# Kernel tuning notes

Hardware: AMD Instinct MI355X
Metric: run time of the kernel (lower is better)

Reference implementation:

```python
import jax, jax.numpy as jnp
import numpy as np

N = 100000

def gcn_conv(x, src, dst, W, b, n):
    # x: [N, Fin]; src/dst: [E'] (self-loops already included); W: [Fin, Fout]
    h = x @ W  # [N, Fout]
    deg = jax.ops.segment_sum(jnp.ones_like(dst, dtype=h.dtype), dst, num_segments=n)  # [N]
    dinv = deg ** -0.5  # deg >= 1 due to self-loops
    norm = dinv[src] * dinv[dst]  # [E']
    msg = h[src] * norm[:, None]  # gather + scale, [E', Fout]
    out = jax.ops.segment_sum(msg, dst, num_segments=n)  # scatter-add to targets
    return out + b

def setup_inputs() -> dict:
    key = jax.random.key(0)
    k1, k2, k3, k4, k5, k6 = jax.random.split(key, 6)
    x = jax.random.normal(k1, (N, 128), dtype=jnp.float32)
    edge_index = jax.random.randint(k2, (2, 1600000), 0, N, dtype=jnp.int32)
    W1 = jax.random.normal(k3, (128, 64), dtype=jnp.float32) * 0.1
    b1 = jnp.zeros((64,), dtype=jnp.float32)
    W2 = jax.random.normal(k4, (64, 41), dtype=jnp.float32) * 0.1
    b2 = jnp.zeros((41,), dtype=jnp.float32)
    return {"x": x, "edge_index": edge_index, "W1": W1, "b1": b1, "W2": W2, "b2": b2}

def reference(x, edge_index, W1, b1, W2, b2):
    n = x.shape[0]
    loops = jnp.arange(n, dtype=edge_index.dtype)
    src = jnp.concatenate([edge_index[0], loops])  # add self-loops (PyG gcn_norm default)
    dst = jnp.concatenate([edge_index[1], loops])
    # dropout is identity in eval mode (self.training=False)
    h = gcn_conv(x, src, dst, W1, b1, n)
    h = jax.nn.relu(h)
    out = gcn_conv(h, src, dst, W2, b2, n)
    return out
```

## Files before the change

kernel.cpp:

```cpp
#include <hip/hip_runtime.h>


#define FIN 128
#define F1  64
#define F2  41
#define FP  64

#define BSH    8
#define BCAP   6144
#define NBMAX  512
#define CHUNK_P 8192

#define MT 128
#define KC 16

__device__ __forceinline__ unsigned short f2bf(float f) {
    unsigned u = __builtin_bit_cast(unsigned, f);
    u += 0x7FFFu + ((u >> 16) & 1u);
    return (unsigned short)(u >> 16);
}
__device__ __forceinline__ float bf2f(unsigned short h) {
    unsigned u = ((unsigned)h) << 16;
    return __builtin_bit_cast(float, u);
}

__global__ void k_zero(int* __restrict__ p, int n) {
    int i = blockIdx.x * blockDim.x + threadIdx.x;
    if (i < n) p[i] = 0;
}

__global__ __launch_bounds__(256) void k_part(
    const int* __restrict__ src, const int* __restrict__ dst,
    int* __restrict__ gcur, int* __restrict__ pairs, int E) {
    __shared__ int hist[NBMAX];
    __shared__ int gsh[NBMAX];
    __shared__ int lex[256];
    __shared__ int limg[CHUNK_P];
    __shared__ int lsh[CHUNK_P];
    __shared__ int stot;
    int tid = threadIdx.x;
    int e0  = blockIdx.x * CHUNK_P;
    hist[tid] = 0; hist[tid + 256] = 0;
    __syncthreads();
    for (int j = 0; j < CHUNK_P / 256; j++) {
        int e = e0 + j * 256 + tid;
        if (e < E) atomicAdd(&hist[dst[e] >> BSH], 1);
    }
    __syncthreads();
    int b0 = 2 * tid, b1 = 2 * tid + 1;
    int c0 = hist[b0], c1 = hist[b1];
    int s  = c0 + c1;
    lex[tid] = s;
    __syncthreads();
    for (int off = 1; off < 256; off <<= 1) {
        int v = lex[tid];
        int a = (tid >= off) ? lex[tid - off] : 0;
        __syncthreads();
        lex[tid] = v + a;
        __syncthreads();
    }
    int incl = lex[tid];
    if (tid == 255) stot = incl;
    int ex = incl - s;
    int l0 = ex, l1 = ex + c0;
    int g0 = c0 ? atomicAdd(&gcur[b0], c0) : 0;
    int g1 = c1 ? atomicAdd(&gcur[b1], c1) : 0;
    hist[b0] = l0; hist[b1] = l1;
    gsh[b0]  = b0 * BCAP + g0 - l0;
    gsh[b1]  = b1 * BCAP + g1 - l1;
    __syncthreads();
    for (int j = 0; j < CHUNK_P / 256; j++) {
        int e = e0 + j * 256 + tid;
        if (e < E) {
            int d = dst[e], sv = src[e];
            int b = d >> BSH;
            int p = atomicAdd(&hist[b], 1);
            limg[p] = (sv << BSH) | (d & 255);
            lsh[p]  = gsh[b];
        }
    }
    __syncthreads();
    int tot = stot;
    for (int k = tid; k < tot; k += 256)
        pairs[k + lsh[k]] = limg[k];
}

__global__ __launch_bounds__(256) void k_build(
    const int* __restrict__ gcur, const int* __restrict__ pairs,
    int* __restrict__ adjcur, int* __restrict__ adj,
    int2* __restrict__ rowinfo, float* __restrict__ dinv, int n) {
    __shared__ int lcnt[256];
    __shared__ int lex[256];
    __shared__ int lcur[256];
    __shared__ int ladj[BCAP];
    __shared__ int sbase;
    int tid = threadIdx.x;
    int b   = blockIdx.x;
    int cntb  = gcur[b]; if (cntb > BCAP) cntb = BCAP;
    int node0 = b << BSH;
    const int* pb = pairs + (size_t)b * BCAP;

    if (tid == 0) sbase = atomicAdd(adjcur, cntb);
    lcnt[tid] = 0;
    __syncthreads();
    for (int k = tid; k < cntb; k += 256) atomicAdd(&lcnt[pb[k] & 255], 1);
    __syncthreads();
    int own = lcnt[tid];
    lex[tid] = own;
    __syncthreads();
    for (int off = 1; off < 256; off <<= 1) {
        int val = lex[tid];
        int add = (tid >= off) ? lex[tid - off] : 0;
        __syncthreads();
        lex[tid] = val + add;
        __syncthreads();
    }
    int excl = lex[tid] - own;
    __syncthreads();
    lex[tid]  = excl;
    lcur[tid] = excl;
    __syncthreads();
    for (int k = tid; k < cntb; k += 256) {
        int pk  = pb[k];
        int pos = atomicAdd(&lcur[pk & 255], 1);
        ladj[pos] = pk >> BSH;
    }
    __syncthreads();
    int base = sbase;
    for (int k = tid; k < cntb; k += 256) adj[base + k] = ladj[k];
    int node = node0 + tid;
    if (node < n) {
        rowinfo[node] = make_int2(base + lex[tid], own);
        dinv[node]    = rsqrtf((float)own + 1.0f);
    }
}

__global__ __launch_bounds__(256) void k_mm1(
    const float* __restrict__ x, const float* __restrict__ W1,
    const float* __restrict__ dinv, unsigned short* __restrict__ hs, int n) {
    __shared__ float Ws[FIN * F1];
    __shared__ float As[KC][MT];
    int t  = threadIdx.x;
    int n0 = blockIdx.x * MT;
#pragma unroll
    for (int j = 0; j < 8; j++) {
        int f = j * 256 + t;
        ((float4*)Ws)[f] = ((const float4*)W1)[f];
    }
    int m0 = (t & 15) * 8;
    int c0 = (t >> 4) * 4;
    int m_l = t & 127;
    int kh  = (t >> 7) * 8;
    bool mvalid = (n0 + m_l) < n;
    const float* xrow = x + (size_t)(n0 + m_l) * FIN + kh;
    float acc[8][4] = {};
    for (int kc = 0; kc < FIN; kc += KC) {
        __syncthreads();
        float4 v0 = mvalid ? *(const float4*)(xrow + kc)     : float4{0.f,0.f,0.f,0.f};
        float4 v1 = mvalid ? *(const float4*)(xrow + kc + 4) : float4{0.f,0.f,0.f,0.f};
        As[kh + 0][m_l] = v0.x; As[kh + 1][m_l] = v0.y;
        As[kh + 2][m_l] = v0.z; As[kh + 3][m_l] = v0.w;
        As[kh + 4][m_l] = v1.x; As[kh + 5][m_l] = v1.y;
        As[kh + 6][m_l] = v1.z; As[kh + 7][m_l] = v1.w;
        __syncthreads();
#pragma unroll
        for (int k = 0; k < KC; k++) {
            float4 a0 = *(const float4*)&As[k][m0];
            float4 a1 = *(const float4*)&As[k][m0 + 4];
            float4 w  = *(const float4*)&Ws[(kc + k) * F1 + c0];
            float a[8] = {a0.x, a0.y, a0.z, a0.w, a1.x, a1.y, a1.z, a1.w};
#pragma unroll
            for (int i = 0; i < 8; i++) {
                acc[i][0] += a[i] * w.x;
                acc[i][1] += a[i] * w.y;
                acc[i][2] += a[i] * w.z;
                acc[i][3] += a[i] * w.w;
            }
        }
    }
#pragma unroll
    for (int i = 0; i < 8; i++) {
        int node = n0 + m0 + i;
        if (node < n) {
            float dv = dinv[node];
            ushort4 o = { f2bf(acc[i][0] * dv), f2bf(acc[i][1] * dv),
                          f2bf(acc[i][2] * dv), f2bf(acc[i][3] * dv) };
            *(ushort4*)&hs[((size_t)node << 6) + c0] = o;
        }
    }
}

__global__ __launch_bounds__(256) void k_agg1(
    const int2* __restrict__ rowinfo, const int* __restrict__ adj,
    const unsigned short* __restrict__ hs, const float* __restrict__ dinv,
    const float* __restrict__ b1, float* __restrict__ h1, int n, int E) {
    int node = blockIdx.x * 4 + (threadIdx.x >> 6);
    if (node >= n) return;
    int lane = threadIdx.x & 63;
    int grp  = lane >> 4;
    int p4   = (lane & 15) * 4;
    int2 ri = rowinfo[node];
    int beg = ri.x, deg = ri.y;
    float4 acc = {0.f, 0.f, 0.f, 0.f};
    if (grp == 0) {
        ushort4 u = *(const ushort4*)&hs[((size_t)node << 6) + p4];
        acc.x = bf2f(u.x); acc.y = bf2f(u.y); acc.z = bf2f(u.z); acc.w = bf2f(u.w);
    }
    for (int base = 0; base < deg; base += 64) {
        int m = deg - base; if (m > 64) m = 64;
        int idx = beg + base + lane;
        int myoff = adj[idx < E ? idx : 0] << 6;
        int e = 0;
        for (; e + 16 <= m; e += 16) {
            int o0 = __shfl(myoff, e + grp),      o1 = __shfl(myoff, e + 4 + grp);
            int o2 = __shfl(myoff, e + 8 + grp),  o3 = __shfl(myoff, e + 12 + grp);
            ushort4 u0 = *(const ushort4*)&hs[(size_t)o0 + p4];
            ushort4 u1 = *(const ushort4*)&hs[(size_t)o1 + p4];
            ushort4 u2 = *(const ushort4*)&hs[(size_t)o2 + p4];
            ushort4 u3 = *(const ushort4*)&hs[(size_t)o3 + p4];
            acc.x += (bf2f(u0.x) + bf2f(u1.x)) + (bf2f(u2.x) + bf2f(u3.x));
            acc.y += (bf2f(u0.y) + bf2f(u1.y)) + (bf2f(u2.y) + bf2f(u3.y));
            acc.z += (bf2f(u0.z) + bf2f(u1.z)) + (bf2f(u2.z) + bf2f(u3.z));
            acc.w += (bf2f(u0.w) + bf2f(u1.w)) + (bf2f(u2.w) + bf2f(u3.w));
        }
        for (; e < m; e += 4) {
            int sl = e + grp;
            int o = __shfl(myoff, sl);
            if (sl < m) {
                ushort4 u = *(const ushort4*)&hs[(size_t)o + p4];
                acc.x += bf2f(u.x); acc.y += bf2f(u.y);
                acc.z += bf2f(u.z); acc.w += bf2f(u.w);
            }
        }
    }
    acc.x += __shfl_xor(acc.x, 16); acc.y += __shfl_xor(acc.y, 16);
    acc.z += __shfl_xor(acc.z, 16); acc.w += __shfl_xor(acc.w, 16);
    acc.x += __shfl_xor(acc.x, 32); acc.y += __shfl_xor(acc.y, 32);
    acc.z += __shfl_xor(acc.z, 32); acc.w += __shfl_xor(acc.w, 32);
    if (grp == 0) {
        float dv = dinv[node];
        float4 bg = *(const float4*)&b1[p4];
        float4 v;
        v.x = acc.x * dv + bg.x; v.x = v.x > 0.f ? v.x : 0.f;
        v.y = acc.y * dv + bg.y; v.y = v.y > 0.f ? v.y : 0.f;
        v.z = acc.z * dv + bg.z; v.z = v.z > 0.f ? v.z : 0.f;
        v.w = acc.w * dv + bg.w; v.w = v.w > 0.f ? v.w : 0.f;
        *(float4*)&h1[((size_t)node << 6) + p4] = v;
    }
}

__global__ __launch_bounds__(256) void k_mm2(
    const float* __restrict__ h1, const float* __restrict__ W2,
    const float* __restrict__ dinv, unsigned short* __restrict__ hs2, int n) {
    __shared__ float Ws[F1 * FP];
    __shared__ float As[KC][MT];
    int t  = threadIdx.x;
    int n0 = blockIdx.x * MT;
    for (int idx = t; idx < F1 * FP; idx += 256) {
        int k = idx >> 6, c = idx & 63;
        Ws[idx] = (c < F2) ? W2[k * F2 + c] : 0.f;
    }
    int m0 = (t & 15) * 8;
    int c0 = (t >> 4) * 4;
    int m_l = t & 127;
    int kh  = (t >> 7) * 8;
    bool mvalid = (n0 + m_l) < n;
    const float* hrow = h1 + (size_t)(n0 + m_l) * F1 + kh;
    float acc[8][4] = {};
    for (int kc = 0; kc < F1; kc += KC) {
        __syncthreads();
        float4 v0 = mvalid ? *(const float4*)(hrow + kc)     : float4{0.f,0.f,0.f,0.f};
        float4 v1 = mvalid ? *(const float4*)(hrow + kc + 4) : float4{0.f,0.f,0.f,0.f};
        As[kh + 0][m_l] = v0.x; As[kh + 1][m_l] = v0.y;
        As[kh + 2][m_l] = v0.z; As[kh + 3][m_l] = v0.w;
        As[kh + 4][m_l] = v1.x; As[kh + 5][m_l] = v1.y;
        As[kh + 6][m_l] = v1.z; As[kh + 7][m_l] = v1.w;
        __syncthreads();
#pragma unroll
        for (int k = 0; k < KC; k++) {
            float4 a0 = *(const float4*)&As[k][m0];
            float4 a1 = *(const float4*)&As[k][m0 + 4];
            float4 w  = *(const float4*)&Ws[(kc + k) * FP + c0];
            float a[8] = {a0.x, a0.y, a0.z, a0.w, a1.x, a1.y, a1.z, a1.w};
#pragma unroll
            for (int i = 0; i < 8; i++) {
                acc[i][0] += a[i] * w.x;
                acc[i][1] += a[i] * w.y;
                acc[i][2] += a[i] * w.z;
                acc[i][3] += a[i] * w.w;
            }
        }
    }
#pragma unroll
    for (int i = 0; i < 8; i++) {
        int node = n0 + m0 + i;
        if (node < n) {
            float dv = dinv[node];
            ushort4 o = { f2bf(acc[i][0] * dv), f2bf(acc[i][1] * dv),
                          f2bf(acc[i][2] * dv), f2bf(acc[i][3] * dv) };
            *(ushort4*)&hs2[((size_t)node << 6) + c0] = o;
        }
    }
}

__global__ __launch_bounds__(256) void k_agg2(
    const int2* __restrict__ rowinfo, const int* __restrict__ adj,
    const unsigned short* __restrict__ hs2, const float* __restrict__ dinv,
    const float* __restrict__ b2, float* __restrict__ out, int n, int E) {
    int node = blockIdx.x * 4 + (threadIdx.x >> 6);
    if (node >= n) return;
    int lane = threadIdx.x & 63;
    int grp  = lane >> 4;
    int p4   = (lane & 15) * 4;
    int2 ri = rowinfo[node];
    int beg = ri.x, deg = ri.y;
    float4 acc = {0.f, 0.f, 0.f, 0.f};
    if (grp == 0) {
        ushort4 u = *(const ushort4*)&hs2[((size_t)node << 6) + p4];
        acc.x = bf2f(u.x); acc.y = bf2f(u.y); acc.z = bf2f(u.z); acc.w = bf2f(u.w);
    }
    for (int base = 0; base < deg; base += 64) {
        int m = deg - base; if (m > 64) m = 64;
        int idx = beg + base + lane;
        int myoff = adj[idx < E ? idx : 0] << 6;
        int e = 0;
        for (; e + 16 <= m; e += 16) {
            int o0 = __shfl(myoff, e + grp),      o1 = __shfl(myoff, e + 4 + grp);
            int o2 = __shfl(myoff, e + 8 + grp),  o3 = __shfl(myoff, e + 12 + grp);
            ushort4 u0 = *(const ushort4*)&hs2[(size_t)o0 + p4];
            ushort4 u1 = *(const ushort4*)&hs2[(size_t)o1 + p4];
            ushort4 u2 = *(const ushort4*)&hs2[(size_t)o2 + p4];
            ushort4 u3 = *(const ushort4*)&hs2[(size_t)o3 + p4];
            acc.x += (bf2f(u0.x) + bf2f(u1.x)) + (bf2f(u2.x) + bf2f(u3.x));
            acc.y += (bf2f(u0.y) + bf2f(u1.y)) + (bf2f(u2.y) + bf2f(u3.y));
            acc.z += (bf2f(u0.z) + bf2f(u1.z)) + (bf2f(u2.z) + bf2f(u3.z));
            acc.w += (bf2f(u0.w) + bf2f(u1.w)) + (bf2f(u2.w) + bf2f(u3.w));
        }
        for (; e < m; e += 4) {
            int sl = e + grp;
            int o = __shfl(myoff, sl);
            if (sl < m) {
                ushort4 u = *(const ushort4*)&hs2[(size_t)o + p4];
                acc.x += bf2f(u.x); acc.y += bf2f(u.y);
                acc.z += bf2f(u.z); acc.w += bf2f(u.w);
            }
        }
    }
    acc.x += __shfl_xor(acc.x, 16); acc.y += __shfl_xor(acc.y, 16);
    acc.z += __shfl_xor(acc.z, 16); acc.w += __shfl_xor(acc.w, 16);
    acc.x += __shfl_xor(acc.x, 32); acc.y += __shfl_xor(acc.y, 32);
    acc.z += __shfl_xor(acc.z, 32); acc.w += __shfl_xor(acc.w, 32);
    if (grp == 0) {
        float dv = dinv[node];
        float vv[4] = {acc.x, acc.y, acc.z, acc.w};
#pragma unroll
        for (int j = 0; j < 4; j++) {
            int f = p4 + j;
            if (f < F2) out[(size_t)node * F2 + f] = vv[j] * dv + b2[f];
        }
    }
}

extern "C" void kernel_launch(void* const* d_in, const int* in_sizes, int n_in,
                              void* d_out, int out_size, void* d_ws, size_t ws_size,
                              hipStream_t stream) {
    const float* x  = (const float*)d_in[0];
    const int*   ei = (const int*)d_in[1];
    const float* W1 = (const float*)d_in[2];
    const float* b1 = (const float*)d_in[3];
    const float* W2 = (const float*)d_in[4];
    const float* b2 = (const float*)d_in[5];
    float* out = (float*)d_out;

    const int n = in_sizes[0] / FIN;
    const int E = in_sizes[1] / 2;
    const int* src = ei;
    const int* dst = ei + E;
    const int nbuck   = (n + 255) >> BSH;
    const int nchunks = (E + CHUNK_P - 1) / CHUNK_P;
    const int nmm     = (n + MT - 1) / MT;
    const int nagg    = (n + 3) / 4;

    char* ws = (char*)d_ws;
    size_t off = 0;
    auto alloc = [&](size_t bytes) {
        void* p = ws + off;
        off = (off + bytes + 511) & ~(size_t)511;
        return p;
    };
    int*   gcur    = (int*)alloc((size_t)(NBMAX + 1) * 4);
    int*   pairs   = (int*)alloc((size_t)nbuck * BCAP * 4);
    int*   adj     = (int*)alloc((size_t)E * 4);
    int2*  rowinfo = (int2*)alloc((size_t)n * 8);
    float* dinv    = (float*)alloc((size_t)n * 4);
    unsigned short* hs1 = (unsigned short*)alloc((size_t)n * FP * 2);
    unsigned short* hs2 = (unsigned short*)alloc((size_t)n * FP * 2);
    float* h1      = (float*)alloc((size_t)n * F1 * 4);

    k_zero<<<(NBMAX + 256) / 256, 256, 0, stream>>>(gcur, NBMAX + 1);
    k_part<<<nchunks, 256, 0, stream>>>(src, dst, gcur, pairs, E);
    k_build<<<nbuck, 256, 0, stream>>>(gcur, pairs, gcur + NBMAX, adj, rowinfo, dinv, n);
    k_mm1<<<nmm, 256, 0, stream>>>(x, W1, dinv, hs1, n);
    k_agg1<<<nagg, 256, 0, stream>>>(rowinfo, adj, hs1, dinv, b1, h1, n, E);
    k_mm2<<<nmm, 256, 0, stream>>>(h1, W2, dinv, hs2, n);
    k_agg2<<<nagg, 256, 0, stream>>>(rowinfo, adj, hs2, dinv, b2, out, n, E);
}
```

Baseline: 293.1 us.

## Sort per-node adjacency, store layer-1 output as bf16, halve partition chunk

```diff
diff --git a/kernel.cpp b/kernel.cpp
--- a/kernel.cpp
+++ b/kernel.cpp
@@ -9,7 +9,7 @@
 #define BSH    8
 #define BCAP   6144
 #define NBMAX  512
-#define CHUNK_P 8192
+#define CHUNK_P 4096
 
 #define MT 128
 #define KC 16
@@ -126,11 +126,24 @@
         ladj[pos] = pk >> BSH;
     }
     __syncthreads();
+    {
+        int s0 = excl;
+        for (int i = 1; i < own; i++) {
+            int key = ladj[s0 + i];
+            int j = i - 1;
+            while (j >= 0 && ladj[s0 + j] > key) {
+                ladj[s0 + j + 1] = ladj[s0 + j];
+                j--;
+            }
+            ladj[s0 + j + 1] = key;
+        }
+    }
+    __syncthreads();
     int base = sbase;
     for (int k = tid; k < cntb; k += 256) adj[base + k] = ladj[k];
     int node = node0 + tid;
     if (node < n) {
-        rowinfo[node] = make_int2(base + lex[tid], own);
+        rowinfo[node] = make_int2(base + excl, own);
         dinv[node]    = rsqrtf((float)own + 1.0f);
     }
 }
@@ -193,7 +206,7 @@
 __global__ __launch_bounds__(256) void k_agg1(
     const int2* __restrict__ rowinfo, const int* __restrict__ adj,
     const unsigned short* __restrict__ hs, const float* __restrict__ dinv,
-    const float* __restrict__ b1, float* __restrict__ h1, int n, int E) {
+    const float* __restrict__ b1, unsigned short* __restrict__ h1b, int n, int E) {
     int node = blockIdx.x * 4 + (threadIdx.x >> 6);
     if (node >= n) return;
     int lane = threadIdx.x & 63;
@@ -240,17 +253,17 @@
     if (grp == 0) {
         float dv = dinv[node];
         float4 bg = *(const float4*)&b1[p4];
-        float4 v;
-        v.x = acc.x * dv + bg.x; v.x = v.x > 0.f ? v.x : 0.f;
-        v.y = acc.y * dv + bg.y; v.y = v.y > 0.f ? v.y : 0.f;
-        v.z = acc.z * dv + bg.z; v.z = v.z > 0.f ? v.z : 0.f;
-        v.w = acc.w * dv + bg.w; v.w = v.w > 0.f ? v.w : 0.f;
-        *(float4*)&h1[((size_t)node << 6) + p4] = v;
+        float vx = acc.x * dv + bg.x; vx = vx > 0.f ? vx : 0.f;
+        float vy = acc.y * dv + bg.y; vy = vy > 0.f ? vy : 0.f;
+        float vz = acc.z * dv + bg.z; vz = vz > 0.f ? vz : 0.f;
+        float vw = acc.w * dv + bg.w; vw = vw > 0.f ? vw : 0.f;
+        ushort4 o = { f2bf(vx), f2bf(vy), f2bf(vz), f2bf(vw) };
+        *(ushort4*)&h1b[((size_t)node << 6) + p4] = o;
     }
 }
 
 __global__ __launch_bounds__(256) void k_mm2(
-    const float* __restrict__ h1, const float* __restrict__ W2,
+    const unsigned short* __restrict__ h1b, const float* __restrict__ W2,
     const float* __restrict__ dinv, unsigned short* __restrict__ hs2, int n) {
     __shared__ float Ws[F1 * FP];
     __shared__ float As[KC][MT];
@@ -265,16 +278,16 @@
     int m_l = t & 127;
     int kh  = (t >> 7) * 8;
     bool mvalid = (n0 + m_l) < n;
-    const float* hrow = h1 + (size_t)(n0 + m_l) * F1 + kh;
+    const unsigned short* hrow = h1b + ((size_t)(n0 + m_l) << 6) + kh;
     float acc[8][4] = {};
     for (int kc = 0; kc < F1; kc += KC) {
         __syncthreads();
-        float4 v0 = mvalid ? *(const float4*)(hrow + kc)     : float4{0.f,0.f,0.f,0.f};
-        float4 v1 = mvalid ? *(const float4*)(hrow + kc + 4) : float4{0.f,0.f,0.f,0.f};
-        As[kh + 0][m_l] = v0.x; As[kh + 1][m_l] = v0.y;
-        As[kh + 2][m_l] = v0.z; As[kh + 3][m_l] = v0.w;
-        As[kh + 4][m_l] = v1.x; As[kh + 5][m_l] = v1.y;
-        As[kh + 6][m_l] = v1.z; As[kh + 7][m_l] = v1.w;
+        ushort4 u0 = mvalid ? *(const ushort4*)(hrow + kc)     : ushort4{0,0,0,0};
+        ushort4 u1 = mvalid ? *(const ushort4*)(hrow + kc + 4) : ushort4{0,0,0,0};
+        As[kh + 0][m_l] = bf2f(u0.x); As[kh + 1][m_l] = bf2f(u0.y);
+        As[kh + 2][m_l] = bf2f(u0.z); As[kh + 3][m_l] = bf2f(u0.w);
+        As[kh + 4][m_l] = bf2f(u1.x); As[kh + 5][m_l] = bf2f(u1.y);
+        As[kh + 6][m_l] = bf2f(u1.z); As[kh + 7][m_l] = bf2f(u1.w);
         __syncthreads();
 #pragma unroll
         for (int k = 0; k < KC; k++) {
@@ -395,13 +408,13 @@
     float* dinv    = (float*)alloc((size_t)n * 4);
     unsigned short* hs1 = (unsigned short*)alloc((size_t)n * FP * 2);
     unsigned short* hs2 = (unsigned short*)alloc((size_t)n * FP * 2);
-    float* h1      = (float*)alloc((size_t)n * F1 * 4);
+    unsigned short* h1b = (unsigned short*)alloc((size_t)n * FP * 2);
 
     k_zero<<<(NBMAX + 256) / 256, 256, 0, stream>>>(gcur, NBMAX + 1);
     k_part<<<nchunks, 256, 0, stream>>>(src, dst, gcur, pairs, E);
     k_build<<<nbuck, 256, 0, stream>>>(gcur, pairs, gcur + NBMAX, adj, rowinfo, dinv, n);
     k_mm1<<<nmm, 256, 0, stream>>>(x, W1, dinv, hs1, n);
-    k_agg1<<<nagg, 256, 0, stream>>>(rowinfo, adj, hs1, dinv, b1, h1, n, E);
-    k_mm2<<<nmm, 256, 0, stream>>>(h1, W2, dinv, hs2, n);
+    k_agg1<<<nagg, 256, 0, stream>>>(rowinfo, adj, hs1, dinv, b1, h1b, n, E);
+    k_mm2<<<nmm, 256, 0, stream>>>(h1b, W2, dinv, hs2, n);
     k_agg2<<<nagg, 256, 0, stream>>>(rowinfo, adj, hs2, dinv, b2, out, n, E);
 }
```

New measurement: 336.0 us. 1.15x slower.
